# Kernel tuning notes

Measured on AMD Instinct MI355X. Metric: run time of the kernel, lower is better.

Reference implementation:

```python
import jax, jax.numpy as jnp
import numpy as np

B, L = 1, 2048
D_MODEL, D_STATE, D_CONV, EXPAND = 512, 16, 4, 2
D_INNER = D_MODEL * EXPAND
EPS = 1e-10  # clamp used by the torch reference


def setup_inputs() -> dict:
    key = jax.random.key(0)
    ks = jax.random.split(key, 8)
    s = lambda fan: 1.0 / np.sqrt(fan)
    x = jax.random.normal(ks[0], (B, L, D_MODEL), jnp.float32)
    # Weights stored in (in, out) layout: y = x @ W  (equivalent to torch Linear with W.T)
    W_in = jax.random.normal(ks[1], (D_MODEL, 2 * D_INNER), jnp.float32) * s(D_MODEL)
    conv_w = jax.random.normal(ks[2], (D_INNER, 1, D_CONV), jnp.float32) * s(D_CONV)  # depthwise (O, I/groups, K)
    conv_b = jax.random.normal(ks[3], (D_INNER,), jnp.float32) * 0.01
    W_xproj = jax.random.normal(ks[4], (D_INNER, 2 * D_STATE + 1), jnp.float32) * s(D_INNER)
    dt_w = jax.random.normal(ks[5], (D_INNER,), jnp.float32) * 0.1  # Linear(1, d_inner) weight, squeezed
    dt_b = jax.random.normal(ks[6], (D_INNER,), jnp.float32) * 0.1 - 2.0  # keep delta smallish
    A_log = jnp.log(jnp.arange(1, D_STATE + 1, dtype=jnp.float32))
    D = jnp.ones((D_INNER,), jnp.float32)
    W_out = jax.random.normal(ks[7], (D_INNER, D_MODEL), jnp.float32) * s(D_INNER)
    return {"x": x, "W_in": W_in, "conv_w": conv_w, "conv_b": conv_b,
            "W_xproj": W_xproj, "dt_w": dt_w, "dt_b": dt_b,
            "A_log": A_log, "D": D, "W_out": W_out}


def reference(x, W_in, conv_w, conv_b, W_xproj, dt_w, dt_b, A_log, D, W_out):
    d_inner, _, d_conv = conv_w.shape
    d_state = A_log.shape[0]

    xz = x @ W_in                                    # (B, L, 2*d_inner)
    xs, z = jnp.split(xz, 2, axis=-1)

    # Depthwise causal conv1d: left-pad d_conv-1 == torch pad-both + truncate to L
    xc = jnp.transpose(xs, (0, 2, 1))                # (B, d_inner, L)
    xc = jax.lax.conv_general_dilated(
        xc, conv_w, window_strides=(1,), padding=[(d_conv - 1, 0)],
        feature_group_count=d_inner,
        dimension_numbers=("NCH", "OIH", "NCH")) + conv_b[None, :, None]
    xs = jax.nn.silu(jnp.transpose(xc, (0, 2, 1)))   # (B, L, d_inner)

    xp = xs @ W_xproj                                # (B, L, 2*d_state+1)
    delta = jax.nn.softplus(xp[..., 0:1] * dt_w + dt_b)  # (B, L, d_inner)
    Bp = xp[..., 1:1 + d_state]                      # (B, L, d_state)
    Cp = xp[..., 1 + d_state:]                       # (B, L, d_state)
    A = -jnp.exp(A_log)                              # (d_state,)

    # --- parallel selective scan via cumulative log-sum (faithful to source) ---
    A_bar = jnp.exp(delta[..., None] * A)                            # (B,L,Di,S)
    BX = delta[..., None] * Bp[:, :, None, :] * xs[..., None]        # (B,L,Di,S)
    log_A_bar = jnp.log(jnp.maximum(A_bar, EPS))
    A_cumsum = jnp.exp(jnp.cumsum(log_A_bar, axis=1))
    A_shift = jnp.concatenate([jnp.ones_like(A_cumsum[:, :1]), A_cumsum[:, :-1]], axis=1)
    weighted_BX = BX / jnp.maximum(A_shift, EPS)
    h = A_cumsum * jnp.cumsum(weighted_BX, axis=1) / jnp.maximum(A_bar, EPS)
    y = jnp.einsum("bls,blds->bld", Cp, h) + D * xs                  # (B,L,Di)

    y = y * jax.nn.silu(z)
    return y @ W_out                                                  # (B,L,D)
```

## Files before the change

kernel.cpp:

```cpp
#include <hip/hip_runtime.h>
#include <hip/hip_bf16.h>


#define L_SEQ 2048
#define DM 512
#define DI 1024
#define DS 16
#define NXP 33
#define EPS 1e-10f
#define RCPEPS 1e10f
#define LOG2E 1.44269504088896340736f
#define LN2 0.69314718055994530942f
#define LOG2EPS -33.219280948873623478f

typedef __hip_bfloat16 bf16;
typedef __attribute__((ext_vector_type(8))) short bf16x8v;
typedef __attribute__((ext_vector_type(4))) float f32x4v;
typedef __attribute__((ext_vector_type(4))) unsigned int u32x4v;

__device__ __forceinline__ float ldf(const float* p) { return *p; }
__device__ __forceinline__ float ldf(const bf16* p) { return __bfloat162float(*p); }

__device__ __forceinline__ void st1(float* p, float v) { *p = v; }
__device__ __forceinline__ void st1(bf16* p, float v) { *p = __float2bfloat16(v); }

__device__ __forceinline__ float fexp2(float x) { return __builtin_amdgcn_exp2f(x); }
__device__ __forceinline__ float frcp(float x) { return __builtin_amdgcn_rcpf(x); }

__device__ __forceinline__ void load8(const float* p, float* v) {
  float4 a = *(const float4*)p;
  float4 b = *(const float4*)(p + 4);
  v[0] = a.x; v[1] = a.y; v[2] = a.z; v[3] = a.w;
  v[4] = b.x; v[5] = b.y; v[6] = b.z; v[7] = b.w;
}
__device__ __forceinline__ void load8(const bf16* p, float* v) {
  bf16 t[8];
  *(uint4*)t = *(const uint4*)p;
#pragma unroll
  for (int j = 0; j < 8; ++j) v[j] = __bfloat162float(t[j]);
}

__global__ __launch_bounds__(256)
void transpose_cast_kernel(const float* __restrict__ W, bf16* __restrict__ WT,
                           int R, int C) {
  __shared__ float tile[32][33];
  int c0 = blockIdx.x * 32, r0 = blockIdx.y * 32;
  int tx = threadIdx.x & 31, ty = threadIdx.x >> 5;
#pragma unroll
  for (int i = 0; i < 4; ++i) {
    int rr = ty + i * 8;
    tile[rr][tx] = W[(size_t)(r0 + rr) * C + c0 + tx];
  }
  __syncthreads();
#pragma unroll
  for (int i = 0; i < 4; ++i) {
    int cc = ty + i * 8;
    WT[(size_t)(c0 + cc) * R + r0 + tx] = __float2bfloat16(tile[tx][cc]);
  }
}

template <typename TA, typename TC>
__global__ __launch_bounds__(256)
void gemm_bt64(const TA* __restrict__ A, const bf16* __restrict__ BT,
               TC* __restrict__ C, int M, int N, int K, int lda, int ldc) {
  __shared__ __align__(16) bf16 As[64 * 40];
  __shared__ __align__(16) bf16 Bs[64 * 40];
  const int tid = threadIdx.x;
  const int wave = tid >> 6, lane = tid & 63;
  const int q = lane >> 4, r = lane & 15;
  const int row0 = blockIdx.y * 64, col0 = blockIdx.x * 64;
  const int srow = tid >> 2, sseg = tid & 3;
  f32x4v acc[4] = {};
  for (int k0 = 0; k0 < K; k0 += 32) {
    {
      float v[8];
      load8(A + (size_t)(row0 + srow) * lda + k0 + sseg * 8, v);
      bf16* dst = &As[srow * 40 + sseg * 8];
#pragma unroll
      for (int j = 0; j < 8; ++j) dst[j] = __float2bfloat16(v[j]);
    }
    *(uint4*)&Bs[srow * 40 + sseg * 8] =
        *(const uint4*)(BT + (size_t)(col0 + srow) * K + k0 + sseg * 8);
    __syncthreads();
    bf16x8v a = *(const bf16x8v*)&As[(wave * 16 + r) * 40 + q * 8];
#pragma unroll
    for (int j = 0; j < 4; ++j) {
      bf16x8v b = *(const bf16x8v*)&Bs[(j * 16 + r) * 40 + q * 8];
      acc[j] = __builtin_amdgcn_mfma_f32_16x16x32_bf16(a, b, acc[j], 0, 0, 0);
    }
    __syncthreads();
  }
#pragma unroll
  for (int j = 0; j < 4; ++j)
#pragma unroll
    for (int reg = 0; reg < 4; ++reg) {
      int m = row0 + wave * 16 + q * 4 + reg;
      int n = col0 + j * 16 + r;
      st1(C + (size_t)m * ldc + n, acc[j][reg]);
    }
}

template <>
__global__ __launch_bounds__(256)
void gemm_bt64<bf16, float>(const bf16* __restrict__ A, const bf16* __restrict__ BT,
                            float* __restrict__ C, int M, int N, int K,
                            int lda, int ldc) {
  __shared__ __align__(16) bf16 As[64 * 40];
  __shared__ __align__(16) bf16 Bs[64 * 40];
  const int tid = threadIdx.x;
  const int wave = tid >> 6, lane = tid & 63;
  const int q = lane >> 4, r = lane & 15;
  const int row0 = blockIdx.y * 64, col0 = blockIdx.x * 64;
  const int srow = tid >> 2, sseg = tid & 3;
  f32x4v acc[4] = {};
  for (int k0 = 0; k0 < K; k0 += 32) {
    *(uint4*)&As[srow * 40 + sseg * 8] =
        *(const uint4*)(A + (size_t)(row0 + srow) * lda + k0 + sseg * 8);
    *(uint4*)&Bs[srow * 40 + sseg * 8] =
        *(const uint4*)(BT + (size_t)(col0 + srow) * K + k0 + sseg * 8);
    __syncthreads();
    bf16x8v a = *(const bf16x8v*)&As[(wave * 16 + r) * 40 + q * 8];
#pragma unroll
    for (int j = 0; j < 4; ++j) {
      bf16x8v b = *(const bf16x8v*)&Bs[(j * 16 + r) * 40 + q * 8];
      acc[j] = __builtin_amdgcn_mfma_f32_16x16x32_bf16(a, b, acc[j], 0, 0, 0);
    }
    __syncthreads();
  }
#pragma unroll
  for (int j = 0; j < 4; ++j)
#pragma unroll
    for (int reg = 0; reg < 4; ++reg) {
      int m = row0 + wave * 16 + q * 4 + reg;
      int n = col0 + j * 16 + r;
      st1(C + (size_t)m * ldc + n, acc[j][reg]);
    }
}

__global__ __launch_bounds__(256)
void gemm_xproj(const bf16* __restrict__ A, const float* __restrict__ Wx,
                float* __restrict__ xpcT) {
  __shared__ __align__(16) bf16 As[64 * 40];
  __shared__ __align__(16) bf16 Bs[64 * 40];
  const int tid = threadIdx.x;
  const int wave = tid >> 6, lane = tid & 63;
  const int q = lane >> 4, r = lane & 15;
  const int row0 = blockIdx.y * 64;
  const int srow = tid >> 2, sseg = tid & 3;
  f32x4v acc[4] = {};
  for (int k0 = 0; k0 < DI; k0 += 32) {
    *(uint4*)&As[srow * 40 + sseg * 8] =
        *(const uint4*)(A + (size_t)(row0 + srow) * DI + k0 + sseg * 8);
    int k = tid >> 3, n0 = (tid & 7) * 8;
#pragma unroll
    for (int j = 0; j < 8; ++j) {
      int n = n0 + j;
      float v = (n < NXP) ? Wx[(size_t)(k0 + k) * NXP + n] : 0.f;
      Bs[n * 40 + k] = __float2bfloat16(v);
    }
    __syncthreads();
    bf16x8v a = *(const bf16x8v*)&As[(wave * 16 + r) * 40 + q * 8];
#pragma unroll
    for (int j = 0; j < 4; ++j) {
      bf16x8v b = *(const bf16x8v*)&Bs[(j * 16 + r) * 40 + q * 8];
      acc[j] = __builtin_amdgcn_mfma_f32_16x16x32_bf16(a, b, acc[j], 0, 0, 0);
    }
    __syncthreads();
  }
#pragma unroll
  for (int j = 0; j < 4; ++j)
#pragma unroll
    for (int reg = 0; reg < 4; ++reg) {
      int m = row0 + wave * 16 + q * 4 + reg;
      int n = j * 16 + r;
      if (n < NXP) xpcT[(size_t)n * L_SEQ + m] = acc[j][reg];
    }
}

__global__ __launch_bounds__(256)
void conv_silu_dual(const bf16* __restrict__ xz, const float* __restrict__ conv_w,
                    const float* __restrict__ conv_b, bf16* __restrict__ xs,
                    bf16* __restrict__ xsT) {
  __shared__ bf16 tile[67][72];
  __shared__ bf16 sout[64][72];
  const int tid = threadIdx.x;
  const int d0 = blockIdx.x * 64, l0 = blockIdx.y * 64;
  for (int slot = tid; slot < 67 * 8; slot += 256) {
    int rr = slot >> 3, seg = slot & 7;
    int l = l0 - 3 + rr;
    uint4 v = {0, 0, 0, 0};
    if (l >= 0) v = *(const uint4*)(xz + (size_t)l * (2 * DI) + d0 + seg * 8);
    *(uint4*)&tile[rr][seg * 8] = v;
  }
  __syncthreads();
  {
    int lr = tid >> 3, c0t = (tid & 7) * 8;
#pragma unroll
    for (int half = 0; half < 2; ++half) {
      int lrow = lr + half * 32;
      bf16 o[8];
#pragma unroll
      for (int j = 0; j < 8; ++j) {
        int c = c0t + j;
        float acc = conv_b[d0 + c];
#pragma unroll
        for (int k = 0; k < 4; ++k)
          acc = fmaf(__bfloat162float(tile[lrow + k][c]), conv_w[(d0 + c) * 4 + k], acc);
        float v = acc / (1.f + __expf(-acc));
        o[j] = __float2bfloat16(v);
        sout[c][lrow] = o[j];
      }
      *(uint4*)(xs + (size_t)(l0 + lrow) * DI + d0 + c0t) = *(uint4*)o;
    }
  }
  __syncthreads();
  for (int slot = tid; slot < 64 * 8; slot += 256) {
    int dd = slot >> 3, seg = slot & 7;
    *(uint4*)(xsT + (size_t)(d0 + dd) * L_SEQ + l0 + seg * 8) =
        *(uint4*)&sout[dd][seg * 8];
  }
}

__global__ __launch_bounds__(256)
void gate_transpose_kernel(const bf16* __restrict__ yT, const bf16* __restrict__ zbuf,
                           int ldz, bf16* __restrict__ ys) {
  __shared__ bf16 tile[64][72];
  int d0 = blockIdx.y * 64, l0 = blockIdx.x * 64;
#pragma unroll
  for (int it = 0; it < 2; ++it) {
    int slot = threadIdx.x + it * 256;
    int dd = slot >> 3, seg = slot & 7;
    *(uint4*)&tile[dd][seg * 8] = *(const uint4*)(yT + (size_t)(d0 + dd) * L_SEQ + l0 + seg * 8);
  }
  __syncthreads();
#pragma unroll
  for (int it = 0; it < 2; ++it) {
    int slot = threadIdx.x + it * 256;
    int ll = slot >> 3, seg = slot & 7;
    bf16 zt[8];
    *(uint4*)zt = *(const uint4*)(zbuf + (size_t)(l0 + ll) * ldz + d0 + seg * 8);
    bf16 o[8];
#pragma unroll
    for (int j = 0; j < 8; ++j) {
      float yv = __bfloat162float(tile[seg * 8 + j][ll]);
      float zv = __bfloat162float(zt[j]);
      o[j] = __float2bfloat16(yv * zv * frcp(1.f + fexp2(-zv * LOG2E)));
    }
    *(uint4*)(ys + (size_t)(l0 + ll) * DI + d0 + seg * 8) = *(uint4*)o;
  }
}

#define LC 512
#define NW 16
#define SPW 32
#define PSX 513
#define LCP 516

__global__ __launch_bounds__(1024)
void scan_kernel(bf16* __restrict__ xsT, const float* __restrict__ xpcT,
                 const float* __restrict__ dt_w, const float* __restrict__ dt_b,
                 const float* __restrict__ A_log, const float* __restrict__ Dvec) {
  __shared__ float sxpT[NXP * PSX];
  __shared__ float sdt[4 * LCP], sg[4 * LCP], sxs[4 * LCP];
  __shared__ float sys[4 * LCP];
  __shared__ float Wtot[NW][64], Vtot[NW][64];
  const int tid = threadIdx.x;
  const int wave = tid >> 6, lane = tid & 63;
  const int s = lane & 15, dl = lane >> 4;
  const int d0 = blockIdx.x * 4;
  const int base = wave * SPW;
  const float As2 = -expf(A_log[s]) * LOG2E;
  const float Dd = Dvec[d0 + dl];
  float dtw[4], dtb[4];
#pragma unroll
  for (int c = 0; c < 4; ++c) {
    dtw[c] = dt_w[d0 + c];
    dtb[c] = dt_b[d0 + c];
  }
  float cs2_carry = 0.f, S_carry = 0.f;
  for (int l0 = 0; l0 < L_SEQ; l0 += LC) {
    for (int idx = tid; idx < NXP * LC; idx += 1024) {
      int j = idx >> 9, l = idx & (LC - 1);
      sxpT[j * PSX + l] = xpcT[(size_t)j * L_SEQ + l0 + l];
    }
    for (int slot = tid; slot < 4 * (LC / 8); slot += 1024) {
      int c = slot >> 6, seg = slot & 63;
      bf16 tmp[8];
      *(uint4*)tmp = *(const uint4*)(xsT + (size_t)(d0 + c) * L_SEQ + l0 + seg * 8);
#pragma unroll
      for (int j = 0; j < 8; ++j) sxs[c * LCP + seg * 8 + j] = __bfloat162float(tmp[j]);
    }
    __syncthreads();
    for (int i = tid; i < LC; i += 1024) {
      float x0 = sxpT[i];
#pragma unroll
      for (int c = 0; c < 4; ++c) {
        float a = fmaf(x0, dtw[c], dtb[c]);
        float dt = __log2f(1.f + fexp2(a * LOG2E)) * LN2;
        sdt[c * LCP + i] = dt;
        sg[c * LCP + i] = dt * sxs[c * LCP + i];
      }
    }
    __syncthreads();
    float P[SPW];
    float Wl = 0.f;
#pragma unroll
    for (int k = 0; k < SPW; ++k) {
      float u = sdt[dl * LCP + base + k] * As2;
      P[k] = Wl;
      Wl += fmaxf(u, LOG2EPS);
    }
    Wtot[wave][lane] = Wl;
    __syncthreads();
    float O = cs2_carry, Wall = 0.f;
    for (int w = 0; w < NW; ++w) {
      float t = Wtot[w][lane];
      if (w < wave) O += t;
      Wall += t;
    }
    float Vl = 0.f;
#pragma unroll
    for (int k = 0; k < SPW; ++k) {
      float rcpA = fminf(fexp2(-(O + P[k])), RCPEPS);
      float gb = sg[dl * LCP + base + k] * sxpT[(1 + s) * PSX + base + k];
      Vl = fmaf(gb, rcpA, Vl);
    }
    Vtot[wave][lane] = Vl;
    __syncthreads();
    float SO = S_carry, Vall = 0.f;
    for (int w = 0; w < NW; ++w) {
      float t = Vtot[w][lane];
      if (w < wave) SO += t;
      Vall += t;
    }
    float S = SO;
#pragma unroll
    for (int k = 0; k < SPW; ++k) {
      float xk = O + P[k];
      float rcpA = fminf(fexp2(-xk), RCPEPS);
      float aprev = fexp2(xk);
      float gb = sg[dl * LCP + base + k] * sxpT[(1 + s) * PSX + base + k];
      S = fmaf(gb, rcpA, S);
      float h = aprev * S;
      float contrib = sxpT[(17 + s) * PSX + base + k] * h;
      contrib += __shfl_xor(contrib, 8);
      contrib += __shfl_xor(contrib, 4);
      contrib += __shfl_xor(contrib, 2);
      contrib += __shfl_xor(contrib, 1);
      if (s == 0)
        sys[dl * LCP + base + k] = contrib + Dd * sxs[dl * LCP + base + k];
    }
    cs2_carry += Wall;
    S_carry += Vall;
    __syncthreads();
    for (int slot = tid; slot < 4 * (LC / 8); slot += 1024) {
      int c = slot >> 6, seg = slot & 63;
      bf16 tmp[8];
#pragma unroll
      for (int j = 0; j < 8; ++j) tmp[j] = __float2bfloat16(sys[c * LCP + seg * 8 + j]);
      u32x4v vv;
      vv.x = ((unsigned int*)tmp)[0]; vv.y = ((unsigned int*)tmp)[1];
      vv.z = ((unsigned int*)tmp)[2]; vv.w = ((unsigned int*)tmp)[3];
      __builtin_nontemporal_store(vv,
          (u32x4v*)(xsT + (size_t)(d0 + c) * L_SEQ + l0 + seg * 8));
    }
    __syncthreads();
  }
}

extern "C" void kernel_launch(void* const* d_in, const int* in_sizes, int n_in,
                              void* d_out, int out_size, void* d_ws, size_t ws_size,
                              hipStream_t stream) {
  const float* x       = (const float*)d_in[0];
  const float* W_in    = (const float*)d_in[1];
  const float* conv_w  = (const float*)d_in[2];
  const float* conv_b  = (const float*)d_in[3];
  const float* W_xproj = (const float*)d_in[4];
  const float* dt_w    = (const float*)d_in[5];
  const float* dt_b    = (const float*)d_in[6];
  const float* A_log   = (const float*)d_in[7];
  const float* Dvec    = (const float*)d_in[8];
  const float* W_out   = (const float*)d_in[9];
  float* out = (float*)d_out;

  char* ws = (char*)d_ws;
  const size_t MB = 1024 * 1024;
  bf16* xz    = (bf16*)(ws);
  bf16* buf1  = (bf16*)(ws + 8 * MB);
  bf16* WinT  = (bf16*)(ws + 12 * MB);
  bf16* xsT   = (bf16*)(ws + 12 * MB);
  bf16* WoutT = (bf16*)(ws + 12 * MB);
  float* xpcT = (float*)(ws + 16 * MB);

  transpose_cast_kernel<<<dim3(2 * DI / 32, DM / 32), 256, 0, stream>>>(
      W_in, WinT, DM, 2 * DI);
  gemm_bt64<float, bf16><<<dim3(2 * DI / 64, L_SEQ / 64), 256, 0, stream>>>(
      x, WinT, xz, L_SEQ, 2 * DI, DM, DM, 2 * DI);
  conv_silu_dual<<<dim3(DI / 64, L_SEQ / 64), 256, 0, stream>>>(
      xz, conv_w, conv_b, buf1, xsT);
  gemm_xproj<<<dim3(1, L_SEQ / 64), 256, 0, stream>>>(buf1, W_xproj, xpcT);
  scan_kernel<<<DI / 4, 1024, 0, stream>>>(xsT, xpcT, dt_w, dt_b, A_log, Dvec);
  gate_transpose_kernel<<<dim3(L_SEQ / 64, DI / 64), 256, 0, stream>>>(
      xsT, xz + DI, 2 * DI, buf1);
  transpose_cast_kernel<<<dim3(DM / 32, DI / 32), 256, 0, stream>>>(
      W_out, WoutT, DI, DM);
  gemm_bt64<bf16, float><<<dim3(DM / 64, L_SEQ / 64), 256, 0, stream>>>(
      buf1, WoutT, out, L_SEQ, DM, DI, DI, DM);
}
```

Measured before the change: 215.8 us.

## Pre-cast input to bf16, use direct global-to-LDS loads in scan, widen dt loop

Adds a separate kernel that casts x to bf16 once, so the input GEMM reads bf16 instead of converting fp32 per tile, and folds the two GEMM variants into one template using if constexpr. In the scan kernel, xpcT is staged with global_load_lds instead of register round-trips, the softplus/dt loop is spread across all 1024 threads instead of 512, and the trailing barrier per chunk is removed. The extra cast kernel adds a launch and a round trip through memory. Removing the barrier risks a race on the shared buffers, and the async LDS loads rely on the existing barrier for visibility.

```diff
diff --git a/kernel.cpp b/kernel.cpp
--- a/kernel.cpp
+++ b/kernel.cpp
@@ -56,6 +56,20 @@
   for (int i = 0; i < 4; ++i) {
     int cc = ty + i * 8;
     WT[(size_t)(c0 + cc) * R + r0 + tx] = __float2bfloat16(tile[tx][cc]);
+  }
+}
+
+__global__ __launch_bounds__(256)
+void cast_f32_bf16_kernel(const float* __restrict__ src, bf16* __restrict__ dst,
+                          int n8) {
+  int i = blockIdx.x * 256 + threadIdx.x;
+  if (i < n8) {
+    float v[8];
+    load8(src + (size_t)i * 8, v);
+    bf16 o[8];
+#pragma unroll
+    for (int j = 0; j < 8; ++j) o[j] = __float2bfloat16(v[j]);
+    *(uint4*)(dst + (size_t)i * 8) = *(uint4*)o;
   }
 }
 
@@ -72,50 +86,16 @@
   const int srow = tid >> 2, sseg = tid & 3;
   f32x4v acc[4] = {};
   for (int k0 = 0; k0 < K; k0 += 32) {
-    {
+    if constexpr (sizeof(TA) == 2) {
+      *(uint4*)&As[srow * 40 + sseg * 8] =
+          *(const uint4*)(A + (size_t)(row0 + srow) * lda + k0 + sseg * 8);
+    } else {
       float v[8];
       load8(A + (size_t)(row0 + srow) * lda + k0 + sseg * 8, v);
       bf16* dst = &As[srow * 40 + sseg * 8];
 #pragma unroll
       for (int j = 0; j < 8; ++j) dst[j] = __float2bfloat16(v[j]);
     }
-    *(uint4*)&Bs[srow * 40 + sseg * 8] =
-        *(const uint4*)(BT + (size_t)(col0 + srow) * K + k0 + sseg * 8);
-    __syncthreads();
-    bf16x8v a = *(const bf16x8v*)&As[(wave * 16 + r) * 40 + q * 8];
-#pragma unroll
-    for (int j = 0; j < 4; ++j) {
-      bf16x8v b = *(const bf16x8v*)&Bs[(j * 16 + r) * 40 + q * 8];
-      acc[j] = __builtin_amdgcn_mfma_f32_16x16x32_bf16(a, b, acc[j], 0, 0, 0);
-    }
-    __syncthreads();
-  }
-#pragma unroll
-  for (int j = 0; j < 4; ++j)
-#pragma unroll
-    for (int reg = 0; reg < 4; ++reg) {
-      int m = row0 + wave * 16 + q * 4 + reg;
-      int n = col0 + j * 16 + r;
-      st1(C + (size_t)m * ldc + n, acc[j][reg]);
-    }
-}
-
-template <>
-__global__ __launch_bounds__(256)
-void gemm_bt64<bf16, float>(const bf16* __restrict__ A, const bf16* __restrict__ BT,
-                            float* __restrict__ C, int M, int N, int K,
-                            int lda, int ldc) {
-  __shared__ __align__(16) bf16 As[64 * 40];
-  __shared__ __align__(16) bf16 Bs[64 * 40];
-  const int tid = threadIdx.x;
-  const int wave = tid >> 6, lane = tid & 63;
-  const int q = lane >> 4, r = lane & 15;
-  const int row0 = blockIdx.y * 64, col0 = blockIdx.x * 64;
-  const int srow = tid >> 2, sseg = tid & 3;
-  f32x4v acc[4] = {};
-  for (int k0 = 0; k0 < K; k0 += 32) {
-    *(uint4*)&As[srow * 40 + sseg * 8] =
-        *(const uint4*)(A + (size_t)(row0 + srow) * lda + k0 + sseg * 8);
     *(uint4*)&Bs[srow * 40 + sseg * 8] =
         *(const uint4*)(BT + (size_t)(col0 + srow) * K + k0 + sseg * 8);
     __syncthreads();
@@ -280,8 +260,12 @@
   float cs2_carry = 0.f, S_carry = 0.f;
   for (int l0 = 0; l0 < L_SEQ; l0 += LC) {
     for (int idx = tid; idx < NXP * LC; idx += 1024) {
-      int j = idx >> 9, l = idx & (LC - 1);
-      sxpT[j * PSX + l] = xpcT[(size_t)j * L_SEQ + l0 + l];
+      int u = __builtin_amdgcn_readfirstlane(idx & ~63);
+      int j = u >> 9, lb = u & (LC - 1);
+      const float* gp = xpcT + (size_t)j * L_SEQ + l0 + lb + lane;
+      __builtin_amdgcn_global_load_lds(
+          (const __attribute__((address_space(1))) void*)gp,
+          (__attribute__((address_space(3))) void*)&sxpT[j * PSX + lb], 4, 0, 0);
     }
     for (int slot = tid; slot < 4 * (LC / 8); slot += 1024) {
       int c = slot >> 6, seg = slot & 63;
@@ -291,15 +275,13 @@
       for (int j = 0; j < 8; ++j) sxs[c * LCP + seg * 8 + j] = __bfloat162float(tmp[j]);
     }
     __syncthreads();
-    for (int i = tid; i < LC; i += 1024) {
+    for (int idx = tid; idx < 4 * LC; idx += 1024) {
+      int c = idx >> 9, i = idx & (LC - 1);
       float x0 = sxpT[i];
-#pragma unroll
-      for (int c = 0; c < 4; ++c) {
-        float a = fmaf(x0, dtw[c], dtb[c]);
-        float dt = __log2f(1.f + fexp2(a * LOG2E)) * LN2;
-        sdt[c * LCP + i] = dt;
-        sg[c * LCP + i] = dt * sxs[c * LCP + i];
-      }
+      float a = fmaf(x0, dtw[c], dtb[c]);
+      float dt = __log2f(1.f + fexp2(a * LOG2E)) * LN2;
+      sdt[c * LCP + i] = dt;
+      sg[c * LCP + i] = dt * sxs[c * LCP + i];
     }
     __syncthreads();
     float P[SPW];
@@ -329,9 +311,9 @@
     __syncthreads();
     float SO = S_carry, Vall = 0.f;
     for (int w = 0; w < NW; ++w) {
-      float t = Vtot[w][lane];
-      if (w < wave) SO += t;
-      Vall += t;
+      float tv = Vtot[w][lane];
+      if (w < wave) SO += tv;
+      Vall += tv;
     }
     float S = SO;
 #pragma unroll
@@ -364,7 +346,6 @@
       __builtin_nontemporal_store(vv,
           (u32x4v*)(xsT + (size_t)(d0 + c) * L_SEQ + l0 + seg * 8));
     }
-    __syncthreads();
   }
 }
 
@@ -388,14 +369,17 @@
   bf16* xz    = (bf16*)(ws);
   bf16* buf1  = (bf16*)(ws + 8 * MB);
   bf16* WinT  = (bf16*)(ws + 12 * MB);
+  bf16* xbf   = (bf16*)(ws + 14 * MB);
   bf16* xsT   = (bf16*)(ws + 12 * MB);
   bf16* WoutT = (bf16*)(ws + 12 * MB);
   float* xpcT = (float*)(ws + 16 * MB);
 
   transpose_cast_kernel<<<dim3(2 * DI / 32, DM / 32), 256, 0, stream>>>(
       W_in, WinT, DM, 2 * DI);
-  gemm_bt64<float, bf16><<<dim3(2 * DI / 64, L_SEQ / 64), 256, 0, stream>>>(
-      x, WinT, xz, L_SEQ, 2 * DI, DM, DM, 2 * DI);
+  cast_f32_bf16_kernel<<<dim3(L_SEQ * DM / (256 * 8)), 256, 0, stream>>>(
+      x, xbf, L_SEQ * DM / 8);
+  gemm_bt64<bf16, bf16><<<dim3(2 * DI / 64, L_SEQ / 64), 256, 0, stream>>>(
+      xbf, WinT, xz, L_SEQ, 2 * DI, DM, DM, 2 * DI);
   conv_silu_dual<<<dim3(DI / 64, L_SEQ / 64), 256, 0, stream>>>(
       xz, conv_w, conv_b, buf1, xsT);
   gemm_xproj<<<dim3(1, L_SEQ / 64), 256, 0, stream>>>(buf1, W_xproj, xpcT);
```

Result: slower. 221.4 us (+2.6%).
